# Kernel tuning notes

Hardware: AMD Instinct MI355X
Metric: run time of the kernel (lower is better)

Reference implementation:

```python
import jax, jax.numpy as jnp
import numpy as np

NUM_CLASSES = 100000
NUM_SAMPLED = 1000
DIM = 512
BATCH = 8192


def _log_uniform_expected_count(ids, num_sampled, range_max):
    # TF LogUniformCandidateSampler: p(c) = (log(c+2) - log(c+1)) / log(range_max+1)
    c = ids.astype(jnp.float32)
    p = (jnp.log(c + 2.0) - jnp.log(c + 1.0)) / jnp.log(float(range_max) + 1.0)
    # expected count under unique sampling with num_sampled tries
    return -jnp.expm1(num_sampled * jnp.log1p(-p))


def setup_inputs() -> dict:
    key = jax.random.key(0)
    k1, k2, k3, k4, k5 = jax.random.split(key, 5)
    y_true = jax.random.randint(k1, (BATCH, 1), 0, NUM_CLASSES, dtype=jnp.int32)
    y_pred = jax.random.normal(k2, (BATCH, DIM), dtype=jnp.float32)
    # learned params sized per init_kwargs (VarianceScaling ~ small uniform; scale only)
    limit = np.sqrt(6.0 / (NUM_CLASSES + DIM))
    W = jax.random.uniform(k3, (NUM_CLASSES, DIM), jnp.float32, -limit, limit)
    b = jax.random.uniform(k4, (NUM_CLASSES,), jnp.float32, -limit, limit)
    sampled = jax.random.randint(k5, (NUM_SAMPLED,), 0, NUM_CLASSES, dtype=jnp.int32)
    return {"y_true": y_true, "y_pred": y_pred, "W": W, "b": b, "sampled": sampled}


def reference(y_true, y_pred, W, b, sampled):
    V = W.shape[0]
    S = sampled.shape[0]
    labels = y_true[:, 0]  # [B], num_true = 1

    # true-class logits: gather rows + batched dot
    w_true = W[labels]                                      # [B, D]
    true_logits = jnp.einsum('bd,bd->b', y_pred, w_true) + b[labels]
    true_logits = true_logits - jnp.log(_log_uniform_expected_count(labels, S, V))

    # sampled-class logits: gather rows + GEMM
    w_s = W[sampled]                                        # [S, D]
    sampled_logits = y_pred @ w_s.T + b[sampled]            # [B, S]
    sampled_logits = sampled_logits - jnp.log(_log_uniform_expected_count(sampled, S, V))

    # remove accidental hits (sampled id == true label)
    hit = labels[:, None] == sampled[None, :]               # [B, S]
    sampled_logits = jnp.where(hit, sampled_logits - 1e9, sampled_logits)

    # softmax cross-entropy with true class at column 0
    logits = jnp.concatenate([true_logits[:, None], sampled_logits], axis=1)  # [B, S+1]
    per_example = jax.nn.logsumexp(logits, axis=1) - logits[:, 0]
    return jnp.mean(per_example)
```

## Files before the change

### kernel.cpp

```cpp
#include <hip/hip_runtime.h>
#include <hip/hip_bf16.h>
#include <math.h>

#define S_SAMPLED 1000
#define SPAD      1024
#define DIM       512
#define BATCH     8192

#define BM 128
#define BN 128
#define BKT 64
#define KTILES (DIM / BKT)
#define NCHUNK 8
#define GEMM_BLOCKS 512
#define FIN_BLOCKS 8
#define M0C 20.0f

typedef __attribute__((ext_vector_type(8))) short short8_t;
typedef __attribute__((ext_vector_type(4))) float f32x4_t;

__device__ __forceinline__ float neg_log_expected(int c) {
    const float log_vp1 = 11.5129354649f;
    float p = log1pf(1.0f / (float)(c + 1)) / log_vp1;
    float E = -expm1f((float)S_SAMPLED * log1pf(-p));
    return -logf(E);
}

__device__ __forceinline__ unsigned short f2bf(float x) {
    __hip_bfloat16 h = __float2bfloat16(x);
    union { __hip_bfloat16 h; unsigned short u; } cv; cv.h = h; return cv.u;
}

__device__ __forceinline__ float b2f(short u) {
    union { float f; unsigned u; } c;
    c.u = ((unsigned)(unsigned short)u) << 16;
    return c.f;
}

__device__ __forceinline__ void load_lds16(const void* g, void* l) {
    __builtin_amdgcn_global_load_lds(
        (const __attribute__((address_space(1))) void*)g,
        (__attribute__((address_space(3))) void*)l, 16, 0, 0);
}

__device__ __forceinline__ int swz(int lin) { return lin ^ (((lin >> 7) & 7) << 4); }

__global__ __launch_bounds__(256) void prep_kernel(
    const float* __restrict__ y_pred, const float* __restrict__ W,
    const float* __restrict__ b, const int* __restrict__ sampled,
    unsigned short* __restrict__ Wg, float* __restrict__ adj,
    unsigned short* __restrict__ ypredB, int* __restrict__ counter)
{
    int bid = blockIdx.x;
    if (bid == 0 && threadIdx.x == 0) *counter = 0;
    if (bid < 512) {
        int row = bid * 2 + (threadIdx.x >> 7);
        int t   = threadIdx.x & 127;
        if (t == 0) {
            if (row < S_SAMPLED) {
                int c = sampled[row];
                adj[row] = b[c] + neg_log_expected(c);
            } else adj[row] = -1e30f;
        }
        unsigned short* dst = Wg + (size_t)row * DIM + t * 4;
        if (row < S_SAMPLED) {
            float4 f = *(const float4*)(W + (size_t)sampled[row] * DIM + t * 4);
            ushort4 o;
            o.x = f2bf(f.x); o.y = f2bf(f.y); o.z = f2bf(f.z); o.w = f2bf(f.w);
            *(ushort4*)dst = o;
        } else {
            *(ushort4*)dst = make_ushort4(0, 0, 0, 0);
        }
    } else {
        int i = (bid - 512) * 2048 + threadIdx.x * 8;
        float4 f0 = *(const float4*)(y_pred + i);
        float4 f1 = *(const float4*)(y_pred + i + 4);
        uint4 o;
        o.x = (unsigned)f2bf(f0.x) | ((unsigned)f2bf(f0.y) << 16);
        o.y = (unsigned)f2bf(f0.z) | ((unsigned)f2bf(f0.w) << 16);
        o.z = (unsigned)f2bf(f1.x) | ((unsigned)f2bf(f1.y) << 16);
        o.w = (unsigned)f2bf(f1.z) | ((unsigned)f2bf(f1.w) << 16);
        *(uint4*)(ypredB + i) = o;
    }
}

__global__ __launch_bounds__(512, 4) void gemm_partial_kernel(
    const unsigned short* __restrict__ Abf,
    const unsigned short* __restrict__ Wg,
    const int*   __restrict__ sampled,
    const float* __restrict__ adj,
    const int*   __restrict__ y_true,
    const float* __restrict__ W,
    const float* __restrict__ b,
    float*       __restrict__ true_v,
    float*       __restrict__ psum)
{
    __shared__ __align__(16) char smem[65536 + 1024];
    char* As0 = smem;
    char* As1 = smem + 16384;
    char* Bs0 = smem + 32768;
    char* Bs1 = smem + 49152;
    float* reds = (float*)(smem + 65536);

    int wg = blockIdx.x;
    int sw = (wg & 7) * 64 + (wg >> 3);
    const int m0    = (sw >> 3) * BM;
    const int chunk = sw & 7;
    const int n0    = chunk * BN;

    const int tid  = threadIdx.x;
    const int lane = tid & 63;
    const int wid  = tid >> 6;
    const int wr   = wid >> 1;
    const int wc   = wid & 1;
    const int g    = lane >> 4;
    const int lcol = lane & 15;

    const char* AB = (const char*)Abf;
    const char* WB = (const char*)Wg;

    int a_src[2], b_src[2];
#pragma unroll
    for (int it = 0; it < 2; ++it) {
        int d = it * 8192 + tid * 16;
        int row = d >> 7;
        int kb  = (d & 127) ^ ((row & 7) << 4);
        a_src[it] = (m0 + row) * (DIM * 2) + kb;
        b_src[it] = (n0 + row) * (DIM * 2) + kb;
    }

    int a_roff[2][2], b_roff[4][2];
#pragma unroll
    for (int mi = 0; mi < 2; ++mi)
#pragma unroll
        for (int ks = 0; ks < 2; ++ks)
            a_roff[mi][ks] = swz((wr * 32 + mi * 16 + lcol) * 128 + ks * 64 + g * 16);
#pragma unroll
    for (int nj = 0; nj < 4; ++nj)
#pragma unroll
        for (int ks = 0; ks < 2; ++ks)
            b_roff[nj][ks] = swz((wc * 64 + nj * 16 + lcol) * 128 + ks * 64 + g * 16);

    f32x4_t acc[2][4] = {};

#define STAGE(AsP, BsP, kt) do {                                     \
        int kb_ = (kt) * 128;                                        \
        load_lds16(AB + a_src[0] + kb_, (AsP) + tid * 16);           \
        load_lds16(AB + a_src[1] + kb_, (AsP) + 8192 + tid * 16);    \
        load_lds16(WB + b_src[0] + kb_, (BsP) + tid * 16);           \
        load_lds16(WB + b_src[1] + kb_, (BsP) + 8192 + tid * 16);    \
    } while (0)

#define COMPUTE(AsP, BsP) do {                                                        \
        _Pragma("unroll")                                                             \
        for (int ks = 0; ks < 2; ++ks) {                                              \
            short8_t a0 = *(const short8_t*)((AsP) + a_roff[0][ks]);                  \
            short8_t a1 = *(const short8_t*)((AsP) + a_roff[1][ks]);                  \
            _Pragma("unroll")                                                         \
            for (int nj = 0; nj < 4; ++nj) {                                          \
                short8_t bv = *(const short8_t*)((BsP) + b_roff[nj][ks]);             \
                acc[0][nj] = __builtin_amdgcn_mfma_f32_16x16x32_bf16(a0, bv, acc[0][nj], 0, 0, 0); \
                acc[1][nj] = __builtin_amdgcn_mfma_f32_16x16x32_bf16(a1, bv, acc[1][nj], 0, 0, 0); \
            }                                                                         \
        }                                                                             \
    } while (0)

    __builtin_amdgcn_sched_barrier(0);
    STAGE(As0, Bs0, 0);
    STAGE(As1, Bs1, 1);
#pragma unroll
    for (int t = 0; t < KTILES; ++t) {
        if (t < KTILES - 1) asm volatile("s_waitcnt vmcnt(4)" ::: "memory");
        else                asm volatile("s_waitcnt vmcnt(0)" ::: "memory");
        __builtin_amdgcn_s_barrier();
        __builtin_amdgcn_sched_barrier(0);
        const char* AsP = (t & 1) ? As1 : As0;
        const char* BsP = (t & 1) ? Bs1 : Bs0;
        __builtin_amdgcn_s_setprio(1);
        COMPUTE(AsP, BsP);
        __builtin_amdgcn_s_setprio(0);
        __builtin_amdgcn_sched_barrier(0);
        __builtin_amdgcn_s_barrier();
        if (t + 2 < KTILES) STAGE((t & 1) ? As1 : As0, (t & 1) ? Bs1 : Bs0, t + 2);
    }
    __builtin_amdgcn_sched_barrier(0);

#pragma unroll
    for (int rr = 0; rr < 2; ++rr) {
        int row = m0 + chunk * 16 + wid * 2 + rr;
        int lab = y_true[row];
        short8_t a8 = *(const short8_t*)(Abf + (size_t)row * DIM + lane * 8);
        float4 w0 = *(const float4*)(W + (size_t)lab * DIM + lane * 8);
        float4 w1 = *(const float4*)(W + (size_t)lab * DIM + lane * 8 + 4);
        float s = b2f(a8[0]) * w0.x + b2f(a8[1]) * w0.y
                + b2f(a8[2]) * w0.z + b2f(a8[3]) * w0.w
                + b2f(a8[4]) * w1.x + b2f(a8[5]) * w1.y
                + b2f(a8[6]) * w1.z + b2f(a8[7]) * w1.w;
#pragma unroll
        for (int off = 32; off; off >>= 1) s += __shfl_xor(s, off);
        if (lane == 0) true_v[row] = s + b[lab] + neg_log_expected(lab);
    }

    int   labs[2][4];
    float srow[2][4];
#pragma unroll
    for (int mi = 0; mi < 2; ++mi)
#pragma unroll
        for (int r = 0; r < 4; ++r) {
            labs[mi][r] = y_true[m0 + wr * 32 + mi * 16 + g * 4 + r];
            srow[mi][r] = 0.f;
        }

    float ajv[4]; int scv[4];
#pragma unroll
    for (int nj = 0; nj < 4; ++nj) {
        int cg = n0 + wc * 64 + nj * 16 + lcol;
        ajv[nj] = adj[cg];
        scv[nj] = (cg < S_SAMPLED) ? sampled[cg] : -2147483647;
    }

#pragma unroll
    for (int mi = 0; mi < 2; ++mi)
#pragma unroll
        for (int nj = 0; nj < 4; ++nj) {
#pragma unroll
            for (int r = 0; r < 4; ++r) {
                float x = acc[mi][nj][r] + ajv[nj];
                if (scv[nj] == labs[mi][r]) x -= 1e9f;
                srow[mi][r] += expf(x - M0C);
            }
        }

#pragma unroll
    for (int s = 1; s < 16; s <<= 1)
#pragma unroll
        for (int mi = 0; mi < 2; ++mi)
#pragma unroll
            for (int r = 0; r < 4; ++r)
                srow[mi][r] += __shfl_xor(srow[mi][r], s);
    if (lcol == 0) {
#pragma unroll
        for (int mi = 0; mi < 2; ++mi)
#pragma unroll
            for (int r = 0; r < 4; ++r)
                reds[wc * 128 + wr * 32 + mi * 16 + g * 4 + r] = srow[mi][r];
    }
    __syncthreads();

    if (tid < BM)
        psum[(size_t)(m0 + tid) * NCHUNK + chunk] = reds[tid] + reds[128 + tid];
#undef STAGE
#undef COMPUTE
}

__global__ __launch_bounds__(1024) void finalize_kernel(
    const float* __restrict__ psum, const float* __restrict__ true_v,
    float* __restrict__ partial, int* __restrict__ counter,
    float* __restrict__ out)
{
    __shared__ float sm[1024];
    __shared__ int s_last;
    int r = blockIdx.x * 1024 + threadIdx.x;
    float4 p0 = *(const float4*)(psum + (size_t)r * NCHUNK);
    float4 p1 = *(const float4*)(psum + (size_t)r * NCHUNK + 4);
    float t = true_v[r];
    float s = p0.x + p0.y + p0.z + p0.w
            + p1.x + p1.y + p1.z + p1.w + expf(t - M0C);
    sm[threadIdx.x] = logf(s) + M0C - t;
    __syncthreads();
    for (int st = 512; st; st >>= 1) {
        if (threadIdx.x < st) sm[threadIdx.x] += sm[threadIdx.x + st];
        __syncthreads();
    }
    if (threadIdx.x == 0) {
        partial[blockIdx.x] = sm[0];
        __threadfence();
        int old = atomicAdd(counter, 1);
        s_last = (old == FIN_BLOCKS - 1) ? 1 : 0;
    }
    __syncthreads();
    if (!s_last || threadIdx.x != 0) return;
    __threadfence();
    float tot = 0.f;
#pragma unroll
    for (int i = 0; i < FIN_BLOCKS; ++i) tot += partial[i];
    out[0] = tot / (float)BATCH;
}

extern "C" void kernel_launch(void* const* d_in, const int* in_sizes, int n_in,
                              void* d_out, int out_size, void* d_ws, size_t ws_size,
                              hipStream_t stream) {
    const int*   y_true  = (const int*)d_in[0];
    const float* y_pred  = (const float*)d_in[1];
    const float* W       = (const float*)d_in[2];
    const float* b       = (const float*)d_in[3];
    const int*   sampled = (const int*)d_in[4];

    char* ws = (char*)d_ws;
    unsigned short* ypredB = (unsigned short*)ws;
    unsigned short* Wg     = (unsigned short*)(ws + 8388608);
    float* adj     = (float*)(ws + 9437184);
    float* true_v  = (float*)(ws + 9441280);
    float* psum    = (float*)(ws + 9474048);
    float* partial = (float*)(ws + 9736192);
    int*   counter = (int*)(ws + 9736256);

    prep_kernel<<<2560, 256, 0, stream>>>(y_pred, W, b, sampled,
                                          Wg, adj, ypredB, counter);
    gemm_partial_kernel<<<GEMM_BLOCKS, 512, 0, stream>>>(
        ypredB, Wg, sampled, adj, y_true, W, b, true_v, psum);
    finalize_kernel<<<FIN_BLOCKS, 1024, 0, stream>>>(
        psum, true_v, partial, counter, (float*)d_out);
}
```

Before: 33.63 us.

## Fuse y_pred bf16 conversion into GEMM and retile to 64x256 tiles

Removes the separate pass that converted y_pred to bf16 in the prep kernel. The GEMM now streams fp32 y_pred straight into LDS and converts it to bf16 in registers before the MFMA. The tile shape changes to 64 rows by 256 columns with K-step 32, using 256-thread blocks and 4 column chunks, and the true-logit dot product now runs in full fp32. The aim is to cut the 8 MB of extra writes and reads plus a prep launch's worth of work. In exchange the fp32 A operand doubles LDS traffic per element, adds conversion ALU work in the inner loop, and leaves fewer threads per block.

```diff
diff --git a/kernel.cpp b/kernel.cpp
--- a/kernel.cpp
+++ b/kernel.cpp
@@ -7,11 +7,11 @@
 #define DIM       512
 #define BATCH     8192
 
-#define BM 128
-#define BN 128
-#define BKT 64
+#define BM 64
+#define BN 256
+#define BKT 32
 #define KTILES (DIM / BKT)
-#define NCHUNK 8
+#define NCHUNK 4
 #define GEMM_BLOCKS 512
 #define FIN_BLOCKS 8
 #define M0C 20.0f
@@ -31,10 +31,13 @@
     union { __hip_bfloat16 h; unsigned short u; } cv; cv.h = h; return cv.u;
 }
 
-__device__ __forceinline__ float b2f(short u) {
-    union { float f; unsigned u; } c;
-    c.u = ((unsigned)(unsigned short)u) << 16;
-    return c.f;
+__device__ __forceinline__ short8_t cvt8(f32x4_t lo, f32x4_t hi) {
+    short8_t r;
+    r[0] = (short)f2bf(lo[0]); r[1] = (short)f2bf(lo[1]);
+    r[2] = (short)f2bf(lo[2]); r[3] = (short)f2bf(lo[3]);
+    r[4] = (short)f2bf(hi[0]); r[5] = (short)f2bf(hi[1]);
+    r[6] = (short)f2bf(hi[2]); r[7] = (short)f2bf(hi[3]);
+    return r;
 }
 
 __device__ __forceinline__ void load_lds16(const void* g, void* l) {
@@ -43,49 +46,35 @@
         (__attribute__((address_space(3))) void*)l, 16, 0, 0);
 }
 
-__device__ __forceinline__ int swz(int lin) { return lin ^ (((lin >> 7) & 7) << 4); }
-
 __global__ __launch_bounds__(256) void prep_kernel(
-    const float* __restrict__ y_pred, const float* __restrict__ W,
-    const float* __restrict__ b, const int* __restrict__ sampled,
+    const float* __restrict__ W, const float* __restrict__ b,
+    const int* __restrict__ sampled,
     unsigned short* __restrict__ Wg, float* __restrict__ adj,
-    unsigned short* __restrict__ ypredB, int* __restrict__ counter)
+    int* __restrict__ counter)
 {
     int bid = blockIdx.x;
     if (bid == 0 && threadIdx.x == 0) *counter = 0;
-    if (bid < 512) {
-        int row = bid * 2 + (threadIdx.x >> 7);
-        int t   = threadIdx.x & 127;
-        if (t == 0) {
-            if (row < S_SAMPLED) {
-                int c = sampled[row];
-                adj[row] = b[c] + neg_log_expected(c);
-            } else adj[row] = -1e30f;
-        }
-        unsigned short* dst = Wg + (size_t)row * DIM + t * 4;
+    int row = bid * 2 + (threadIdx.x >> 7);
+    int t   = threadIdx.x & 127;
+    if (t == 0) {
         if (row < S_SAMPLED) {
-            float4 f = *(const float4*)(W + (size_t)sampled[row] * DIM + t * 4);
-            ushort4 o;
-            o.x = f2bf(f.x); o.y = f2bf(f.y); o.z = f2bf(f.z); o.w = f2bf(f.w);
-            *(ushort4*)dst = o;
-        } else {
-            *(ushort4*)dst = make_ushort4(0, 0, 0, 0);
-        }
+            int c = sampled[row];
+            adj[row] = b[c] + neg_log_expected(c);
+        } else adj[row] = -1e30f;
+    }
+    unsigned short* dst = Wg + (size_t)row * DIM + t * 4;
+    if (row < S_SAMPLED) {
+        float4 f = *(const float4*)(W + (size_t)sampled[row] * DIM + t * 4);
+        ushort4 o;
+        o.x = f2bf(f.x); o.y = f2bf(f.y); o.z = f2bf(f.z); o.w = f2bf(f.w);
+        *(ushort4*)dst = o;
     } else {
-        int i = (bid - 512) * 2048 + threadIdx.x * 8;
-        float4 f0 = *(const float4*)(y_pred + i);
-        float4 f1 = *(const float4*)(y_pred + i + 4);
-        uint4 o;
-        o.x = (unsigned)f2bf(f0.x) | ((unsigned)f2bf(f0.y) << 16);
-        o.y = (unsigned)f2bf(f0.z) | ((unsigned)f2bf(f0.w) << 16);
-        o.z = (unsigned)f2bf(f1.x) | ((unsigned)f2bf(f1.y) << 16);
-        o.w = (unsigned)f2bf(f1.z) | ((unsigned)f2bf(f1.w) << 16);
-        *(uint4*)(ypredB + i) = o;
-    }
-}
-
-__global__ __launch_bounds__(512, 4) void gemm_partial_kernel(
-    const unsigned short* __restrict__ Abf,
+        *(ushort4*)dst = make_ushort4(0, 0, 0, 0);
+    }
+}
+
+__global__ __launch_bounds__(256, 3) void gemm_partial_kernel(
+    const float* __restrict__ Ay,
     const unsigned short* __restrict__ Wg,
     const int*   __restrict__ sampled,
     const float* __restrict__ adj,
@@ -95,17 +84,17 @@
     float*       __restrict__ true_v,
     float*       __restrict__ psum)
 {
-    __shared__ __align__(16) char smem[65536 + 1024];
+    __shared__ __align__(16) char smem[49152 + 512];
     char* As0 = smem;
-    char* As1 = smem + 16384;
-    char* Bs0 = smem + 32768;
-    char* Bs1 = smem + 49152;
-    float* reds = (float*)(smem + 65536);
+    char* As1 = smem + 8192;
+    char* Bs0 = smem + 16384;
+    char* Bs1 = smem + 32768;
+    float* reds = (float*)(smem + 49152);
 
     int wg = blockIdx.x;
     int sw = (wg & 7) * 64 + (wg >> 3);
-    const int m0    = (sw >> 3) * BM;
-    const int chunk = sw & 7;
+    const int m0    = (sw >> 2) * BM;
+    const int chunk = sw & 3;
     const int n0    = chunk * BN;
 
     const int tid  = threadIdx.x;
@@ -116,52 +105,61 @@
     const int g    = lane >> 4;
     const int lcol = lane & 15;
 
-    const char* AB = (const char*)Abf;
+    const char* AF = (const char*)Ay;
     const char* WB = (const char*)Wg;
 
-    int a_src[2], b_src[2];
+    int a_src[2];
 #pragma unroll
     for (int it = 0; it < 2; ++it) {
-        int d = it * 8192 + tid * 16;
+        int d = it * 4096 + tid * 16;
         int row = d >> 7;
         int kb  = (d & 127) ^ ((row & 7) << 4);
-        a_src[it] = (m0 + row) * (DIM * 2) + kb;
-        b_src[it] = (n0 + row) * (DIM * 2) + kb;
-    }
-
-    int a_roff[2][2], b_roff[4][2];
-#pragma unroll
-    for (int mi = 0; mi < 2; ++mi)
-#pragma unroll
-        for (int ks = 0; ks < 2; ++ks)
-            a_roff[mi][ks] = swz((wr * 32 + mi * 16 + lcol) * 128 + ks * 64 + g * 16);
-#pragma unroll
-    for (int nj = 0; nj < 4; ++nj)
-#pragma unroll
-        for (int ks = 0; ks < 2; ++ks)
-            b_roff[nj][ks] = swz((wc * 64 + nj * 16 + lcol) * 128 + ks * 64 + g * 16);
-
-    f32x4_t acc[2][4] = {};
-
-#define STAGE(AsP, BsP, kt) do {                                     \
-        int kb_ = (kt) * 128;                                        \
-        load_lds16(AB + a_src[0] + kb_, (AsP) + tid * 16);           \
-        load_lds16(AB + a_src[1] + kb_, (AsP) + 8192 + tid * 16);    \
-        load_lds16(WB + b_src[0] + kb_, (BsP) + tid * 16);           \
-        load_lds16(WB + b_src[1] + kb_, (BsP) + 8192 + tid * 16);    \
+        a_src[it] = (m0 + row) * (DIM * 4) + kb;
+    }
+    int b_src[4];
+#pragma unroll
+    for (int it = 0; it < 4; ++it) {
+        int d = it * 4096 + tid * 16;
+        int col = d >> 6;
+        int kb  = (d & 63) ^ ((col & 3) << 4);
+        b_src[it] = (n0 + col) * (DIM * 2) + kb;
+    }
+
+    int a_roff[2], b_roff[8];
+#pragma unroll
+    for (int mi = 0; mi < 2; ++mi) {
+        int r = wr * 32 + mi * 16 + lcol;
+        a_roff[mi] = r * 128 + ((g * 32) ^ ((r & 7) << 4));
+    }
+#pragma unroll
+    for (int nj = 0; nj < 8; ++nj) {
+        int c = wc * 128 + nj * 16 + lcol;
+        b_roff[nj] = c * 64 + ((g * 16) ^ ((c & 3) << 4));
+    }
+
+    f32x4_t acc[2][8] = {};
+
+#define STAGE(AsP, BsP, kt) do {                                       \
+        load_lds16(AF + a_src[0] + (kt) * 128, (AsP) + tid * 16);      \
+        load_lds16(AF + a_src[1] + (kt) * 128, (AsP) + 4096 + tid * 16); \
+        load_lds16(WB + b_src[0] + (kt) * 64, (BsP) + tid * 16);       \
+        load_lds16(WB + b_src[1] + (kt) * 64, (BsP) + 4096 + tid * 16); \
+        load_lds16(WB + b_src[2] + (kt) * 64, (BsP) + 8192 + tid * 16); \
+        load_lds16(WB + b_src[3] + (kt) * 64, (BsP) + 12288 + tid * 16); \
     } while (0)
 
 #define COMPUTE(AsP, BsP) do {                                                        \
+        f32x4_t lo0 = *(const f32x4_t*)((AsP) + a_roff[0]);                           \
+        f32x4_t hi0 = *(const f32x4_t*)((AsP) + (a_roff[0] ^ 16));                    \
+        f32x4_t lo1 = *(const f32x4_t*)((AsP) + a_roff[1]);                           \
+        f32x4_t hi1 = *(const f32x4_t*)((AsP) + (a_roff[1] ^ 16));                    \
+        short8_t a0 = cvt8(lo0, hi0);                                                 \
+        short8_t a1 = cvt8(lo1, hi1);                                                 \
         _Pragma("unroll")                                                             \
-        for (int ks = 0; ks < 2; ++ks) {                                              \
-            short8_t a0 = *(const short8_t*)((AsP) + a_roff[0][ks]);                  \
-            short8_t a1 = *(const short8_t*)((AsP) + a_roff[1][ks]);                  \
-            _Pragma("unroll")                                                         \
-            for (int nj = 0; nj < 4; ++nj) {                                          \
-                short8_t bv = *(const short8_t*)((BsP) + b_roff[nj][ks]);             \
-                acc[0][nj] = __builtin_amdgcn_mfma_f32_16x16x32_bf16(a0, bv, acc[0][nj], 0, 0, 0); \
-                acc[1][nj] = __builtin_amdgcn_mfma_f32_16x16x32_bf16(a1, bv, acc[1][nj], 0, 0, 0); \
-            }                                                                         \
+        for (int nj = 0; nj < 8; ++nj) {                                              \
+            short8_t bv = *(const short8_t*)((BsP) + b_roff[nj]);                     \
+            acc[0][nj] = __builtin_amdgcn_mfma_f32_16x16x32_bf16(a0, bv, acc[0][nj], 0, 0, 0); \
+            acc[1][nj] = __builtin_amdgcn_mfma_f32_16x16x32_bf16(a1, bv, acc[1][nj], 0, 0, 0); \
         }                                                                             \
     } while (0)
 
@@ -170,7 +168,7 @@
     STAGE(As1, Bs1, 1);
 #pragma unroll
     for (int t = 0; t < KTILES; ++t) {
-        if (t < KTILES - 1) asm volatile("s_waitcnt vmcnt(4)" ::: "memory");
+        if (t < KTILES - 1) asm volatile("s_waitcnt vmcnt(6)" ::: "memory");
         else                asm volatile("s_waitcnt vmcnt(0)" ::: "memory");
         __builtin_amdgcn_s_barrier();
         __builtin_amdgcn_sched_barrier(0);
@@ -186,16 +184,15 @@
     __builtin_amdgcn_sched_barrier(0);
 
 #pragma unroll
-    for (int rr = 0; rr < 2; ++rr) {
-        int row = m0 + chunk * 16 + wid * 2 + rr;
+    for (int rr = 0; rr < 4; ++rr) {
+        int row = m0 + chunk * 16 + wid * 4 + rr;
         int lab = y_true[row];
-        short8_t a8 = *(const short8_t*)(Abf + (size_t)row * DIM + lane * 8);
-        float4 w0 = *(const float4*)(W + (size_t)lab * DIM + lane * 8);
-        float4 w1 = *(const float4*)(W + (size_t)lab * DIM + lane * 8 + 4);
-        float s = b2f(a8[0]) * w0.x + b2f(a8[1]) * w0.y
-                + b2f(a8[2]) * w0.z + b2f(a8[3]) * w0.w
-                + b2f(a8[4]) * w1.x + b2f(a8[5]) * w1.y
-                + b2f(a8[6]) * w1.z + b2f(a8[7]) * w1.w;
+        f32x4_t p0 = *(const f32x4_t*)(Ay + (size_t)row * DIM + lane * 8);
+        f32x4_t p1 = *(const f32x4_t*)(Ay + (size_t)row * DIM + lane * 8 + 4);
+        f32x4_t w0 = *(const f32x4_t*)(W + (size_t)lab * DIM + lane * 8);
+        f32x4_t w1 = *(const f32x4_t*)(W + (size_t)lab * DIM + lane * 8 + 4);
+        float s = p0[0] * w0[0] + p0[1] * w0[1] + p0[2] * w0[2] + p0[3] * w0[3]
+                + p1[0] * w1[0] + p1[1] * w1[1] + p1[2] * w1[2] + p1[3] * w1[3];
 #pragma unroll
         for (int off = 32; off; off >>= 1) s += __shfl_xor(s, off);
         if (lane == 0) true_v[row] = s + b[lab] + neg_log_expected(lab);
@@ -211,10 +208,10 @@
             srow[mi][r] = 0.f;
         }
 
-    float ajv[4]; int scv[4];
-#pragma unroll
-    for (int nj = 0; nj < 4; ++nj) {
-        int cg = n0 + wc * 64 + nj * 16 + lcol;
+    float ajv[8]; int scv[8];
+#pragma unroll
+    for (int nj = 0; nj < 8; ++nj) {
+        int cg = n0 + wc * 128 + nj * 16 + lcol;
         ajv[nj] = adj[cg];
         scv[nj] = (cg < S_SAMPLED) ? sampled[cg] : -2147483647;
     }
@@ -222,7 +219,7 @@
 #pragma unroll
     for (int mi = 0; mi < 2; ++mi)
 #pragma unroll
-        for (int nj = 0; nj < 4; ++nj) {
+        for (int nj = 0; nj < 8; ++nj) {
 #pragma unroll
             for (int r = 0; r < 4; ++r) {
                 float x = acc[mi][nj][r] + ajv[nj];
@@ -243,12 +240,12 @@
         for (int mi = 0; mi < 2; ++mi)
 #pragma unroll
             for (int r = 0; r < 4; ++r)
-                reds[wc * 128 + wr * 32 + mi * 16 + g * 4 + r] = srow[mi][r];
+                reds[wc * 64 + wr * 32 + mi * 16 + g * 4 + r] = srow[mi][r];
     }
     __syncthreads();
 
     if (tid < BM)
-        psum[(size_t)(m0 + tid) * NCHUNK + chunk] = reds[tid] + reds[128 + tid];
+        psum[(size_t)(m0 + tid) * NCHUNK + chunk] = reds[tid] + reds[64 + tid];
 #undef STAGE
 #undef COMPUTE
 }
@@ -262,10 +259,8 @@
     __shared__ int s_last;
     int r = blockIdx.x * 1024 + threadIdx.x;
     float4 p0 = *(const float4*)(psum + (size_t)r * NCHUNK);
-    float4 p1 = *(const float4*)(psum + (size_t)r * NCHUNK + 4);
     float t = true_v[r];
-    float s = p0.x + p0.y + p0.z + p0.w
-            + p1.x + p1.y + p1.z + p1.w + expf(t - M0C);
+    float s = p0.x + p0.y + p0.z + p0.w + expf(t - M0C);
     sm[threadIdx.x] = logf(s) + M0C - t;
     __syncthreads();
     for (int st = 512; st; st >>= 1) {
@@ -297,18 +292,16 @@
     const int*   sampled = (const int*)d_in[4];
 
     char* ws = (char*)d_ws;
-    unsigned short* ypredB = (unsigned short*)ws;
-    unsigned short* Wg     = (unsigned short*)(ws + 8388608);
-    float* adj     = (float*)(ws + 9437184);
-    float* true_v  = (float*)(ws + 9441280);
-    float* psum    = (float*)(ws + 9474048);
-    float* partial = (float*)(ws + 9736192);
-    int*   counter = (int*)(ws + 9736256);
-
-    prep_kernel<<<2560, 256, 0, stream>>>(y_pred, W, b, sampled,
-                                          Wg, adj, ypredB, counter);
-    gemm_partial_kernel<<<GEMM_BLOCKS, 512, 0, stream>>>(
-        ypredB, Wg, sampled, adj, y_true, W, b, true_v, psum);
+    unsigned short* Wg = (unsigned short*)ws;
+    float* adj     = (float*)(ws + 1048576);
+    float* true_v  = (float*)(ws + 1052672);
+    float* psum    = (float*)(ws + 1085440);
+    float* partial = (float*)(ws + 1216512);
+    int*   counter = (int*)(ws + 1216576);
+
+    prep_kernel<<<512, 256, 0, stream>>>(W, b, sampled, Wg, adj, counter);
+    gemm_partial_kernel<<<GEMM_BLOCKS, 256, 0, stream>>>(
+        y_pred, Wg, sampled, adj, y_true, W, b, true_v, psum);
     finalize_kernel<<<FIN_BLOCKS, 1024, 0, stream>>>(
         psum, true_v, partial, counter, (float*)d_out);
 }
```

Result: slower. 37.95 us (+12.9%).

## Halve GEMM N-tile to 64 and double grid; coarsen y_pred conversion blocks

Applied to the files above, without the earlier changes.

The GEMM tile width drops from 128 to 64 sampled columns, giving 16 column chunks and 1024 workgroups instead of 512. LDS per block shrinks, and the launch-bound occupancy hint rises from 4 to 6 to fit more waves per CU. The psum layout, finalize reduction, true-logit row assignment and workspace offsets are updated to match. The y_pred bf16 conversion now handles four segments per thread with fewer prep blocks. The aim is better CU fill and latency hiding, at the cost of reloading the A tile twice as often and lower MFMA reuse per B load.

```diff
diff --git a/kernel.cpp b/kernel.cpp
--- a/kernel.cpp
+++ b/kernel.cpp
@@ -8,11 +8,11 @@
 #define BATCH     8192
 
 #define BM 128
-#define BN 128
+#define BN 64
 #define BKT 64
 #define KTILES (DIM / BKT)
-#define NCHUNK 8
-#define GEMM_BLOCKS 512
+#define NCHUNK 16
+#define GEMM_BLOCKS 1024
 #define FIN_BLOCKS 8
 #define M0C 20.0f
 
@@ -72,19 +72,23 @@
             *(ushort4*)dst = make_ushort4(0, 0, 0, 0);
         }
     } else {
-        int i = (bid - 512) * 2048 + threadIdx.x * 8;
-        float4 f0 = *(const float4*)(y_pred + i);
-        float4 f1 = *(const float4*)(y_pred + i + 4);
-        uint4 o;
-        o.x = (unsigned)f2bf(f0.x) | ((unsigned)f2bf(f0.y) << 16);
-        o.y = (unsigned)f2bf(f0.z) | ((unsigned)f2bf(f0.w) << 16);
-        o.z = (unsigned)f2bf(f1.x) | ((unsigned)f2bf(f1.y) << 16);
-        o.w = (unsigned)f2bf(f1.z) | ((unsigned)f2bf(f1.w) << 16);
-        *(uint4*)(ypredB + i) = o;
-    }
-}
-
-__global__ __launch_bounds__(512, 4) void gemm_partial_kernel(
+        int base = (bid - 512) * 8192 + threadIdx.x * 8;
+#pragma unroll
+        for (int h = 0; h < 4; ++h) {
+            int i = base + h * 2048;
+            float4 f0 = *(const float4*)(y_pred + i);
+            float4 f1 = *(const float4*)(y_pred + i + 4);
+            uint4 o;
+            o.x = (unsigned)f2bf(f0.x) | ((unsigned)f2bf(f0.y) << 16);
+            o.y = (unsigned)f2bf(f0.z) | ((unsigned)f2bf(f0.w) << 16);
+            o.z = (unsigned)f2bf(f1.x) | ((unsigned)f2bf(f1.y) << 16);
+            o.w = (unsigned)f2bf(f1.z) | ((unsigned)f2bf(f1.w) << 16);
+            *(uint4*)(ypredB + i) = o;
+        }
+    }
+}
+
+__global__ __launch_bounds__(512, 6) void gemm_partial_kernel(
     const unsigned short* __restrict__ Abf,
     const unsigned short* __restrict__ Wg,
     const int*   __restrict__ sampled,
@@ -95,17 +99,17 @@
     float*       __restrict__ true_v,
     float*       __restrict__ psum)
 {
-    __shared__ __align__(16) char smem[65536 + 1024];
+    __shared__ __align__(16) char smem[49152 + 1024];
     char* As0 = smem;
     char* As1 = smem + 16384;
     char* Bs0 = smem + 32768;
-    char* Bs1 = smem + 49152;
-    float* reds = (float*)(smem + 65536);
+    char* Bs1 = smem + 40960;
+    float* reds = (float*)(smem + 49152);
 
     int wg = blockIdx.x;
-    int sw = (wg & 7) * 64 + (wg >> 3);
-    const int m0    = (sw >> 3) * BM;
-    const int chunk = sw & 7;
+    int sw = (wg & 7) * 128 + (wg >> 3);
+    const int m0    = (sw >> 4) * BM;
+    const int chunk = sw & 15;
     const int n0    = chunk * BN;
 
     const int tid  = threadIdx.x;
@@ -119,36 +123,40 @@
     const char* AB = (const char*)Abf;
     const char* WB = (const char*)Wg;
 
-    int a_src[2], b_src[2];
+    int a_src[2], b_src;
 #pragma unroll
     for (int it = 0; it < 2; ++it) {
         int d = it * 8192 + tid * 16;
         int row = d >> 7;
         int kb  = (d & 127) ^ ((row & 7) << 4);
         a_src[it] = (m0 + row) * (DIM * 2) + kb;
-        b_src[it] = (n0 + row) * (DIM * 2) + kb;
-    }
-
-    int a_roff[2][2], b_roff[4][2];
+    }
+    {
+        int d = tid * 16;
+        int col = d >> 7;
+        int kb  = (d & 127) ^ ((col & 7) << 4);
+        b_src = (n0 + col) * (DIM * 2) + kb;
+    }
+
+    int a_roff[2][2], b_roff[2][2];
 #pragma unroll
     for (int mi = 0; mi < 2; ++mi)
 #pragma unroll
         for (int ks = 0; ks < 2; ++ks)
             a_roff[mi][ks] = swz((wr * 32 + mi * 16 + lcol) * 128 + ks * 64 + g * 16);
 #pragma unroll
-    for (int nj = 0; nj < 4; ++nj)
+    for (int nj = 0; nj < 2; ++nj)
 #pragma unroll
         for (int ks = 0; ks < 2; ++ks)
-            b_roff[nj][ks] = swz((wc * 64 + nj * 16 + lcol) * 128 + ks * 64 + g * 16);
-
-    f32x4_t acc[2][4] = {};
+            b_roff[nj][ks] = swz((wc * 32 + nj * 16 + lcol) * 128 + ks * 64 + g * 16);
+
+    f32x4_t acc[2][2] = {};
 
 #define STAGE(AsP, BsP, kt) do {                                     \
         int kb_ = (kt) * 128;                                        \
         load_lds16(AB + a_src[0] + kb_, (AsP) + tid * 16);           \
         load_lds16(AB + a_src[1] + kb_, (AsP) + 8192 + tid * 16);    \
-        load_lds16(WB + b_src[0] + kb_, (BsP) + tid * 16);           \
-        load_lds16(WB + b_src[1] + kb_, (BsP) + 8192 + tid * 16);    \
+        load_lds16(WB + b_src + kb_, (BsP) + tid * 16);              \
     } while (0)
 
 #define COMPUTE(AsP, BsP) do {                                                        \
@@ -157,7 +165,7 @@
             short8_t a0 = *(const short8_t*)((AsP) + a_roff[0][ks]);                  \
             short8_t a1 = *(const short8_t*)((AsP) + a_roff[1][ks]);                  \
             _Pragma("unroll")                                                         \
-            for (int nj = 0; nj < 4; ++nj) {                                          \
+            for (int nj = 0; nj < 2; ++nj) {                                          \
                 short8_t bv = *(const short8_t*)((BsP) + b_roff[nj][ks]);             \
                 acc[0][nj] = __builtin_amdgcn_mfma_f32_16x16x32_bf16(a0, bv, acc[0][nj], 0, 0, 0); \
                 acc[1][nj] = __builtin_amdgcn_mfma_f32_16x16x32_bf16(a1, bv, acc[1][nj], 0, 0, 0); \
@@ -170,7 +178,7 @@
     STAGE(As1, Bs1, 1);
 #pragma unroll
     for (int t = 0; t < KTILES; ++t) {
-        if (t < KTILES - 1) asm volatile("s_waitcnt vmcnt(4)" ::: "memory");
+        if (t < KTILES - 1) asm volatile("s_waitcnt vmcnt(3)" ::: "memory");
         else                asm volatile("s_waitcnt vmcnt(0)" ::: "memory");
         __builtin_amdgcn_s_barrier();
         __builtin_amdgcn_sched_barrier(0);
@@ -185,9 +193,8 @@
     }
     __builtin_amdgcn_sched_barrier(0);
 
-#pragma unroll
-    for (int rr = 0; rr < 2; ++rr) {
-        int row = m0 + chunk * 16 + wid * 2 + rr;
+    {
+        int row = m0 + chunk * 8 + wid;
         int lab = y_true[row];
         short8_t a8 = *(const short8_t*)(Abf + (size_t)row * DIM + lane * 8);
         float4 w0 = *(const float4*)(W + (size_t)lab * DIM + lane * 8);
@@ -211,10 +218,10 @@
             srow[mi][r] = 0.f;
         }
 
-    float ajv[4]; int scv[4];
-#pragma unroll
-    for (int nj = 0; nj < 4; ++nj) {
-        int cg = n0 + wc * 64 + nj * 16 + lcol;
+    float ajv[2]; int scv[2];
+#pragma unroll
+    for (int nj = 0; nj < 2; ++nj) {
+        int cg = n0 + wc * 32 + nj * 16 + lcol;
         ajv[nj] = adj[cg];
         scv[nj] = (cg < S_SAMPLED) ? sampled[cg] : -2147483647;
     }
@@ -222,7 +229,7 @@
 #pragma unroll
     for (int mi = 0; mi < 2; ++mi)
 #pragma unroll
-        for (int nj = 0; nj < 4; ++nj) {
+        for (int nj = 0; nj < 2; ++nj) {
 #pragma unroll
             for (int r = 0; r < 4; ++r) {
                 float x = acc[mi][nj][r] + ajv[nj];
@@ -261,11 +268,12 @@
     __shared__ float sm[1024];
     __shared__ int s_last;
     int r = blockIdx.x * 1024 + threadIdx.x;
-    float4 p0 = *(const float4*)(psum + (size_t)r * NCHUNK);
-    float4 p1 = *(const float4*)(psum + (size_t)r * NCHUNK + 4);
+    const float4* pp = (const float4*)(psum + (size_t)r * NCHUNK);
+    float4 p0 = pp[0], p1 = pp[1], p2 = pp[2], p3 = pp[3];
     float t = true_v[r];
-    float s = p0.x + p0.y + p0.z + p0.w
-            + p1.x + p1.y + p1.z + p1.w + expf(t - M0C);
+    float s = p0.x + p0.y + p0.z + p0.w + p1.x + p1.y + p1.z + p1.w
+            + p2.x + p2.y + p2.z + p2.w + p3.x + p3.y + p3.z + p3.w
+            + expf(t - M0C);
     sm[threadIdx.x] = logf(s) + M0C - t;
     __syncthreads();
     for (int st = 512; st; st >>= 1) {
@@ -302,10 +310,10 @@
     float* adj     = (float*)(ws + 9437184);
     float* true_v  = (float*)(ws + 9441280);
     float* psum    = (float*)(ws + 9474048);
-    float* partial = (float*)(ws + 9736192);
-    int*   counter = (int*)(ws + 9736256);
-
-    prep_kernel<<<2560, 256, 0, stream>>>(y_pred, W, b, sampled,
+    float* partial = (float*)(ws + 9998336);
+    int*   counter = (int*)(ws + 9998400);
+
+    prep_kernel<<<1024, 256, 0, stream>>>(y_pred, W, b, sampled,
                                           Wg, adj, ypredB, counter);
     gemm_partial_kernel<<<GEMM_BLOCKS, 512, 0, stream>>>(
         ypredB, Wg, sampled, adj, y_true, W, b, true_v, psum);
```

New measurement: 35.66 us. 6.1% more time.

## Switch sampled-logit GEMM from bf16 to scaled fp8 e4m3 MFMA

Applied to the files above, without the earlier changes.

Converts y_pred and the gathered W rows to fp8 e4m3 instead of bf16, scaling W by 64 before quantisation and undoing the scale in the epilogue. The GEMM now uses the fp8 16x16x32 MFMA over 128-wide K tiles, which halves operand bytes and the number of K iterations. The true-class dot product now reads fp32 y_pred directly, and the prep kernel launches fewer, larger conversion blocks. This reduces precision of the sampled logits, which could affect loss accuracy tolerance.

```diff
diff --git a/kernel.cpp b/kernel.cpp
--- a/kernel.cpp
+++ b/kernel.cpp
@@ -9,14 +9,15 @@
 
 #define BM 128
 #define BN 128
-#define BKT 64
+#define BKT 128
 #define KTILES (DIM / BKT)
 #define NCHUNK 8
 #define GEMM_BLOCKS 512
 #define FIN_BLOCKS 8
 #define M0C 20.0f
-
-typedef __attribute__((ext_vector_type(8))) short short8_t;
+#define WSCALE 64.0f
+#define INV_WSCALE 0.015625f
+
 typedef __attribute__((ext_vector_type(4))) float f32x4_t;
 
 __device__ __forceinline__ float neg_log_expected(int c) {
@@ -26,15 +27,19 @@
     return -logf(E);
 }
 
-__device__ __forceinline__ unsigned short f2bf(float x) {
-    __hip_bfloat16 h = __float2bfloat16(x);
-    union { __hip_bfloat16 h; unsigned short u; } cv; cv.h = h; return cv.u;
-}
-
-__device__ __forceinline__ float b2f(short u) {
-    union { float f; unsigned u; } c;
-    c.u = ((unsigned)(unsigned short)u) << 16;
-    return c.f;
+__device__ __forceinline__ unsigned f2e4m3(float x) {
+    unsigned u = __float_as_uint(x);
+    unsigned s = (u >> 24) & 0x80;
+    float ax = fabsf(x);
+    if (ax < 0.015625f) {
+        int m = (int)rintf(ax * 512.0f);
+        return s | (unsigned)m;
+    }
+    unsigned au = u & 0x7fffffffu;
+    unsigned r = au + 0x0007ffffu + ((au >> 20) & 1);
+    int e = (int)(r >> 23) - 120;
+    unsigned m = (r >> 20) & 7;
+    return s | ((unsigned)e << 3) | m;
 }
 
 __device__ __forceinline__ void load_lds16(const void* g, void* l) {
@@ -48,8 +53,8 @@
 __global__ __launch_bounds__(256) void prep_kernel(
     const float* __restrict__ y_pred, const float* __restrict__ W,
     const float* __restrict__ b, const int* __restrict__ sampled,
-    unsigned short* __restrict__ Wg, float* __restrict__ adj,
-    unsigned short* __restrict__ ypredB, int* __restrict__ counter)
+    unsigned char* __restrict__ Wg8, float* __restrict__ adj,
+    unsigned char* __restrict__ ypred8, int* __restrict__ counter)
 {
     int bid = blockIdx.x;
     if (bid == 0 && threadIdx.x == 0) *counter = 0;
@@ -62,34 +67,39 @@
                 adj[row] = b[c] + neg_log_expected(c);
             } else adj[row] = -1e30f;
         }
-        unsigned short* dst = Wg + (size_t)row * DIM + t * 4;
+        unsigned char* dst = Wg8 + (size_t)row * DIM + t * 4;
         if (row < S_SAMPLED) {
             float4 f = *(const float4*)(W + (size_t)sampled[row] * DIM + t * 4);
-            ushort4 o;
-            o.x = f2bf(f.x); o.y = f2bf(f.y); o.z = f2bf(f.z); o.w = f2bf(f.w);
-            *(ushort4*)dst = o;
+            unsigned o = f2e4m3(f.x * WSCALE) | (f2e4m3(f.y * WSCALE) << 8)
+                       | (f2e4m3(f.z * WSCALE) << 16) | (f2e4m3(f.w * WSCALE) << 24);
+            *(unsigned*)dst = o;
         } else {
-            *(ushort4*)dst = make_ushort4(0, 0, 0, 0);
+            *(unsigned*)dst = 0u;
         }
     } else {
-        int i = (bid - 512) * 2048 + threadIdx.x * 8;
-        float4 f0 = *(const float4*)(y_pred + i);
-        float4 f1 = *(const float4*)(y_pred + i + 4);
-        uint4 o;
-        o.x = (unsigned)f2bf(f0.x) | ((unsigned)f2bf(f0.y) << 16);
-        o.y = (unsigned)f2bf(f0.z) | ((unsigned)f2bf(f0.w) << 16);
-        o.z = (unsigned)f2bf(f1.x) | ((unsigned)f2bf(f1.y) << 16);
-        o.w = (unsigned)f2bf(f1.z) | ((unsigned)f2bf(f1.w) << 16);
-        *(uint4*)(ypredB + i) = o;
+        int base = (bid - 512) * 8192 + threadIdx.x * 8;
+#pragma unroll
+        for (int h = 0; h < 4; ++h) {
+            int i = base + h * 2048;
+            float4 f0 = *(const float4*)(y_pred + i);
+            float4 f1 = *(const float4*)(y_pred + i + 4);
+            unsigned lo = f2e4m3(f0.x) | (f2e4m3(f0.y) << 8)
+                        | (f2e4m3(f0.z) << 16) | (f2e4m3(f0.w) << 24);
+            unsigned hi = f2e4m3(f1.x) | (f2e4m3(f1.y) << 8)
+                        | (f2e4m3(f1.z) << 16) | (f2e4m3(f1.w) << 24);
+            *(unsigned long long*)(ypred8 + i) =
+                (unsigned long long)lo | ((unsigned long long)hi << 32);
+        }
     }
 }
 
 __global__ __launch_bounds__(512, 4) void gemm_partial_kernel(
-    const unsigned short* __restrict__ Abf,
-    const unsigned short* __restrict__ Wg,
+    const unsigned char* __restrict__ A8,
+    const unsigned char* __restrict__ Wg8,
     const int*   __restrict__ sampled,
     const float* __restrict__ adj,
     const int*   __restrict__ y_true,
+    const float* __restrict__ y_pred,
     const float* __restrict__ W,
     const float* __restrict__ b,
     float*       __restrict__ true_v,
@@ -116,8 +126,8 @@
     const int g    = lane >> 4;
     const int lcol = lane & 15;
 
-    const char* AB = (const char*)Abf;
-    const char* WB = (const char*)Wg;
+    const char* AB = (const char*)A8;
+    const char* WB = (const char*)Wg8;
 
     int a_src[2], b_src[2];
 #pragma unroll
@@ -125,21 +135,21 @@
         int d = it * 8192 + tid * 16;
         int row = d >> 7;
         int kb  = (d & 127) ^ ((row & 7) << 4);
-        a_src[it] = (m0 + row) * (DIM * 2) + kb;
-        b_src[it] = (n0 + row) * (DIM * 2) + kb;
-    }
-
-    int a_roff[2][2], b_roff[4][2];
+        a_src[it] = (m0 + row) * DIM + kb;
+        b_src[it] = (n0 + row) * DIM + kb;
+    }
+
+    int a_roff[2][4], b_roff[4][4];
 #pragma unroll
     for (int mi = 0; mi < 2; ++mi)
 #pragma unroll
-        for (int ks = 0; ks < 2; ++ks)
-            a_roff[mi][ks] = swz((wr * 32 + mi * 16 + lcol) * 128 + ks * 64 + g * 16);
+        for (int ks = 0; ks < 4; ++ks)
+            a_roff[mi][ks] = swz((wr * 32 + mi * 16 + lcol) * 128 + ks * 32 + g * 8);
 #pragma unroll
     for (int nj = 0; nj < 4; ++nj)
 #pragma unroll
-        for (int ks = 0; ks < 2; ++ks)
-            b_roff[nj][ks] = swz((wc * 64 + nj * 16 + lcol) * 128 + ks * 64 + g * 16);
+        for (int ks = 0; ks < 4; ++ks)
+            b_roff[nj][ks] = swz((wc * 64 + nj * 16 + lcol) * 128 + ks * 32 + g * 8);
 
     f32x4_t acc[2][4] = {};
 
@@ -153,14 +163,14 @@
 
 #define COMPUTE(AsP, BsP) do {                                                        \
         _Pragma("unroll")                                                             \
-        for (int ks = 0; ks < 2; ++ks) {                                              \
-            short8_t a0 = *(const short8_t*)((AsP) + a_roff[0][ks]);                  \
-            short8_t a1 = *(const short8_t*)((AsP) + a_roff[1][ks]);                  \
+        for (int ks = 0; ks < 4; ++ks) {                                              \
+            long a0 = *(const long*)((AsP) + a_roff[0][ks]);                          \
+            long a1 = *(const long*)((AsP) + a_roff[1][ks]);                          \
             _Pragma("unroll")                                                         \
             for (int nj = 0; nj < 4; ++nj) {                                          \
-                short8_t bv = *(const short8_t*)((BsP) + b_roff[nj][ks]);             \
-                acc[0][nj] = __builtin_amdgcn_mfma_f32_16x16x32_bf16(a0, bv, acc[0][nj], 0, 0, 0); \
-                acc[1][nj] = __builtin_amdgcn_mfma_f32_16x16x32_bf16(a1, bv, acc[1][nj], 0, 0, 0); \
+                long bv = *(const long*)((BsP) + b_roff[nj][ks]);                     \
+                acc[0][nj] = __builtin_amdgcn_mfma_f32_16x16x32_fp8_fp8(a0, bv, acc[0][nj], 0, 0, 0); \
+                acc[1][nj] = __builtin_amdgcn_mfma_f32_16x16x32_fp8_fp8(a1, bv, acc[1][nj], 0, 0, 0); \
             }                                                                         \
         }                                                                             \
     } while (0)
@@ -189,13 +199,12 @@
     for (int rr = 0; rr < 2; ++rr) {
         int row = m0 + chunk * 16 + wid * 2 + rr;
         int lab = y_true[row];
-        short8_t a8 = *(const short8_t*)(Abf + (size_t)row * DIM + lane * 8);
-        float4 w0 = *(const float4*)(W + (size_t)lab * DIM + lane * 8);
-        float4 w1 = *(const float4*)(W + (size_t)lab * DIM + lane * 8 + 4);
-        float s = b2f(a8[0]) * w0.x + b2f(a8[1]) * w0.y
-                + b2f(a8[2]) * w0.z + b2f(a8[3]) * w0.w
-                + b2f(a8[4]) * w1.x + b2f(a8[5]) * w1.y
-                + b2f(a8[6]) * w1.z + b2f(a8[7]) * w1.w;
+        f32x4_t p0 = *(const f32x4_t*)(y_pred + (size_t)row * DIM + lane * 8);
+        f32x4_t p1 = *(const f32x4_t*)(y_pred + (size_t)row * DIM + lane * 8 + 4);
+        f32x4_t w0 = *(const f32x4_t*)(W + (size_t)lab * DIM + lane * 8);
+        f32x4_t w1 = *(const f32x4_t*)(W + (size_t)lab * DIM + lane * 8 + 4);
+        float s = p0[0] * w0[0] + p0[1] * w0[1] + p0[2] * w0[2] + p0[3] * w0[3]
+                + p1[0] * w1[0] + p1[1] * w1[1] + p1[2] * w1[2] + p1[3] * w1[3];
 #pragma unroll
         for (int off = 32; off; off >>= 1) s += __shfl_xor(s, off);
         if (lane == 0) true_v[row] = s + b[lab] + neg_log_expected(lab);
@@ -225,7 +234,7 @@
         for (int nj = 0; nj < 4; ++nj) {
 #pragma unroll
             for (int r = 0; r < 4; ++r) {
-                float x = acc[mi][nj][r] + ajv[nj];
+                float x = acc[mi][nj][r] * INV_WSCALE + ajv[nj];
                 if (scv[nj] == labs[mi][r]) x -= 1e9f;
                 srow[mi][r] += expf(x - M0C);
             }
@@ -297,18 +306,18 @@
     const int*   sampled = (const int*)d_in[4];
 
     char* ws = (char*)d_ws;
-    unsigned short* ypredB = (unsigned short*)ws;
-    unsigned short* Wg     = (unsigned short*)(ws + 8388608);
-    float* adj     = (float*)(ws + 9437184);
-    float* true_v  = (float*)(ws + 9441280);
-    float* psum    = (float*)(ws + 9474048);
-    float* partial = (float*)(ws + 9736192);
-    int*   counter = (int*)(ws + 9736256);
-
-    prep_kernel<<<2560, 256, 0, stream>>>(y_pred, W, b, sampled,
-                                          Wg, adj, ypredB, counter);
+    unsigned char* ypred8 = (unsigned char*)ws;
+    unsigned char* Wg8    = (unsigned char*)(ws + 4194304);
+    float* adj     = (float*)(ws + 4718592);
+    float* true_v  = (float*)(ws + 4722688);
+    float* psum    = (float*)(ws + 4755456);
+    float* partial = (float*)(ws + 5017600);
+    int*   counter = (int*)(ws + 5017664);
+
+    prep_kernel<<<1024, 256, 0, stream>>>(y_pred, W, b, sampled,
+                                          Wg8, adj, ypred8, counter);
     gemm_partial_kernel<<<GEMM_BLOCKS, 512, 0, stream>>>(
-        ypredB, Wg, sampled, adj, y_true, W, b, true_v, psum);
+        ypred8, Wg8, sampled, adj, y_true, y_pred, W, b, true_v, psum);
     finalize_kernel<<<FIN_BLOCKS, 1024, 0, stream>>>(
         psum, true_v, partial, counter, (float*)d_out);
 }
```

Result: faster. 31.67 us (-5.8%).
